# Performance work log

Hardware: AMD Instinct MI355X
Metric: run time of the kernel (lower is better)

Reference implementation:

```python
import jax, jax.numpy as jnp
import numpy as np
from jax import lax

B, N, C = 4, 20000, 256
NUM_VIEW = 300
NUM_SAMPLE = 1024
EPS_BN = 1e-5


def _grasp_views(n=NUM_VIEW):
    # graspnetAPI generate_grasp_views: spiral points on unit sphere
    phi = (np.sqrt(5.0) - 1.0) / 2.0
    i = np.arange(n)
    z = (2.0 * i + 1.0) / n - 1.0
    r = np.sqrt(np.maximum(1.0 - z * z, 0.0))
    x = r * np.cos(2.0 * np.pi * i * phi)
    y = r * np.sin(2.0 * np.pi * i * phi)
    return jnp.asarray(np.stack([x, y, z], axis=1).astype(np.float32))  # [300,3]

_TEMPLATE_VIEWS = _grasp_views()


def _conv1x1(x, w, b):
    # Conv1d with kernel_size=1: x [B,Cin,N], w [Cout,Cin], b [Cout]
    return jnp.einsum('oc,bcn->bon', w, x) + b[None, :, None]


def _bn_eval(x, g, be, m, v):
    # BatchNorm1d in eval mode (running stats)
    scale = g / jnp.sqrt(v + EPS_BN)
    return x * scale[None, :, None] + (be - m * scale)[None, :, None]


def _masked_fps(xyz, mask, n_samples):
    # Equivalent to compacting valid points, running torch furthest_point_sample,
    # and mapping indices back: run FPS on the full set with invalid points pinned
    # to -inf min-distance so they are never selected. Start = first valid index
    # (index 0 of the compacted set). Tie-breaking matches (order preserved).
    first = jnp.argmax(mask, axis=1)                      # [B]
    init_d = jnp.where(mask, jnp.float32(1e10), -jnp.inf)  # [B,N]

    def step(carry, _):
        dists, last = carry
        p = jnp.take_along_axis(xyz, last[:, None, None], axis=1)  # [B,1,3]
        d = jnp.sum((xyz - p) ** 2, axis=-1)                       # [B,N]
        dists = jnp.minimum(dists, d)
        nxt = jnp.argmax(dists, axis=1)
        return (dists, nxt), nxt

    _, rest = lax.scan(step, (init_d, first), None, length=n_samples - 1)
    return jnp.concatenate([first[None, :], rest], axis=0).T  # [B,S] int


def _viewpoint_to_matrix(towards):
    # batch_viewpoint_params_to_matrix with batch_angle = 0 => R1 = I
    ax = towards  # [M,3]
    ay = jnp.stack([-ax[:, 1], ax[:, 0], jnp.zeros_like(ax[:, 0])], axis=-1)
    deg = jnp.sum(ay * ay, axis=-1, keepdims=True) == 0
    ay = jnp.where(deg, jnp.array([0.0, 1.0, 0.0], dtype=ax.dtype), ay)
    nx = ax / jnp.linalg.norm(ax, axis=-1, keepdims=True)
    ny = ay / jnp.linalg.norm(ay, axis=-1, keepdims=True)
    nz = jnp.cross(nx, ny)
    return jnp.stack([nx, ny, nz], axis=-1)  # [M,3,3], axes as columns


def setup_inputs() -> dict:
    key = jax.random.key(0)
    ks = jax.random.split(key, 18)

    def w(k, shape, s=0.05):
        return jax.random.normal(k, shape, jnp.float32) * s

    return dict(
        seed_xyz=jax.random.normal(ks[0], (B, N, 3), jnp.float32),
        seed_features=jax.random.normal(ks[1], (B, C, N), jnp.float32),
        gh_w1=w(ks[2], (C, C)), gh_b1=w(ks[3], (C,), 0.01),
        gh_g=1.0 + 0.1 * jax.random.normal(ks[4], (C,), jnp.float32),
        gh_be=w(ks[5], (C,), 0.01),
        gh_m=w(ks[6], (C,), 0.1),
        gh_v=jax.random.uniform(ks[7], (C,), jnp.float32, 0.5, 1.5),
        gh_w2=w(ks[8], (3, C)), gh_b2=w(ks[9], (3,), 0.01),
        c1_w=w(ks[10], (C, C)), c1_b=w(ks[11], (C,), 0.01),
        bn_g=1.0 + 0.1 * jax.random.normal(ks[12], (C,), jnp.float32),
        bn_b=w(ks[13], (C,), 0.01),
        bn_m=w(ks[14], (C,), 0.1),
        bn_v=jax.random.uniform(ks[15], (C,), jnp.float32, 0.5, 1.5),
        c2_w=w(ks[16], (3, C)), c2_b=w(ks[17], (3,), 0.01),
    )


def reference(seed_xyz, seed_features, gh_w1, gh_b1, gh_g, gh_be, gh_m, gh_v,
              gh_w2, gh_b2, c1_w, c1_b, bn_g, bn_b, bn_m, bn_v, c2_w, c2_b):
    # graspable head: conv-BN-ReLU-conv -> [B,3,N]
    h = jax.nn.relu(_bn_eval(_conv1x1(seed_features, gh_w1, gh_b1), gh_g, gh_be, gh_m, gh_v))
    graspable = _conv1x1(h, gh_w2, gh_b2)
    objectness_score = graspable[:, :2]          # [B,2,N]
    graspness_score = graspable[:, 2]            # [B,N]

    obj_mask = jnp.argmax(objectness_score, axis=1) == 1
    gmask = (graspness_score > 0.1) & obj_mask   # [B,N] bool

    graspable_inds = _masked_fps(seed_xyz, gmask, NUM_SAMPLE)            # [B,S]
    graspable_xyz = jnp.take_along_axis(seed_xyz, graspable_inds[:, :, None], axis=1)   # [B,S,3]
    graspable_features = jnp.take_along_axis(seed_features, graspable_inds[:, None, :], axis=2)  # [B,C,S]
    fp2_graspness = jnp.take_along_axis(graspness_score, graspable_inds, axis=1)        # [B,S]

    f = jax.nn.relu(_bn_eval(_conv1x1(graspable_features, c1_w, c1_b), bn_g, bn_b, bn_m, bn_v))
    vp_xyz = jnp.transpose(_conv1x1(f, c2_w, c2_b), (0, 2, 1))  # [B,S,3]

    # cosine similarity against 300 template views (torch clamps each norm at 1e-8)
    vn = vp_xyz / jnp.maximum(jnp.linalg.norm(vp_xyz, axis=-1, keepdims=True), 1e-8)
    tn = _TEMPLATE_VIEWS / jnp.maximum(jnp.linalg.norm(_TEMPLATE_VIEWS, axis=-1, keepdims=True), 1e-8)
    cos = jnp.einsum('bsd,vd->bsv', vn, tn)      # [B,S,300]
    top_view_inds = jnp.argmax(cos, axis=2)      # [B,S]

    vp_rot = _viewpoint_to_matrix(-vp_xyz.reshape(-1, 3)).reshape(B, NUM_SAMPLE, 3, 3)

    return (objectness_score, graspness_score, graspable_xyz, graspable_inds,
            graspable_features, fp2_graspness, vp_xyz, top_view_inds, vp_rot)
```

## Files before the change

kernel.cpp:

```cpp
#include <hip/hip_runtime.h>
#include <hip/hip_bf16.h>
#include <math.h>

static constexpr int BB = 4;
static constexpr int NN = 20000;
static constexpr int CC = 256;
static constexpr int SS = 1024;
static constexpr int NV = 300;

static constexpr size_t O0 = 0;
static constexpr size_t O1 = O0 + (size_t)BB*2*NN;
static constexpr size_t O2 = O1 + (size_t)BB*NN;
static constexpr size_t O3 = O2 + (size_t)BB*SS*3;
static constexpr size_t O4 = O3 + (size_t)BB*SS;
static constexpr size_t O5 = O4 + (size_t)BB*CC*SS;
static constexpr size_t O6 = O5 + (size_t)BB*SS;
static constexpr size_t O7 = O6 + (size_t)BB*SS*3;
static constexpr size_t O8 = O7 + (size_t)BB*SS;

typedef float v2f __attribute__((ext_vector_type(2)));

static constexpr int KC = 32;
static constexpr int SW_LD = 260;
static constexpr int PS_LD = 68;

static constexpr int G1_TN  = 128;
static constexpr int G1_KC  = 16;
static constexpr int G1_LD  = 260;
static constexpr int G1_BUF = G1_KC*G1_LD + G1_KC*G1_TN;

__global__ __launch_bounds__(256, 2) void gemm_fused(
    const float* __restrict__ X,
    const float* __restrict__ W1, const float* __restrict__ B1v,
    const float* __restrict__ Gv, const float* __restrict__ BEv,
    const float* __restrict__ Mv, const float* __restrict__ Vv,
    const float* __restrict__ W2, const float* __restrict__ B2v,
    float* __restrict__ o0, float* __restrict__ o1)
{
    __shared__ alignas(16) float smem[2*G1_BUF];
    float* psum = smem;

    const int t  = threadIdx.x;
    const int b  = blockIdx.y;
    const int n0 = blockIdx.x * G1_TN;
    const int tm = t & 31;
    const int tj = t >> 5;
    const float* Xb = X + (size_t)b * CC * NN;
    const bool full = (n0 + G1_TN <= NN);

    v2f acc2[8][8];
#pragma unroll
    for (int i = 0; i < 8; ++i)
#pragma unroll
        for (int jp = 0; jp < 8; ++jp) acc2[i][jp] = (v2f){0.f, 0.f};

    float4 wreg[4];
    float4 xr0, xr1;

    auto stage_load = [&](int k0) {
#pragma unroll
        for (int r = 0; r < 4; ++r) {
            int f  = r*1024 + t*4;
            int m  = f >> 4;
            int kk = f & 15;
            wreg[r] = *(const float4*)&W1[(size_t)m*CC + k0 + kk];
        }
        int fx = t*8;
        int kk = fx >> 7;
        int j  = fx & 127;
        if (full) {
            xr0 = *(const float4*)&Xb[(size_t)(k0+kk)*NN + n0 + j];
            xr1 = *(const float4*)&Xb[(size_t)(k0+kk)*NN + n0 + j + 4];
        } else {
            float ta[4], tb[4];
#pragma unroll
            for (int u = 0; u < 4; ++u) {
                int c0 = n0 + j + u;
                int c1 = n0 + j + 4 + u;
                ta[u] = (c0 < NN) ? Xb[(size_t)(k0+kk)*NN + c0] : 0.f;
                tb[u] = (c1 < NN) ? Xb[(size_t)(k0+kk)*NN + c1] : 0.f;
            }
            xr0 = make_float4(ta[0], ta[1], ta[2], ta[3]);
            xr1 = make_float4(tb[0], tb[1], tb[2], tb[3]);
        }
    };

    auto stage_write = [&](float* base) {
        float* sWb = base;
        float* sFb = base + G1_KC*G1_LD;
#pragma unroll
        for (int r = 0; r < 4; ++r) {
            int f  = r*1024 + t*4;
            int m  = f >> 4;
            int kk = f & 15;
            float tmp[4] = {wreg[r].x, wreg[r].y, wreg[r].z, wreg[r].w};
#pragma unroll
            for (int u = 0; u < 4; ++u)
                sWb[(kk+u)*G1_LD + m] = tmp[u];
        }
        int fx = t*8;
        int kk = fx >> 7;
        int j  = fx & 127;
        *(float4*)&sFb[kk*G1_TN + j]     = xr0;
        *(float4*)&sFb[kk*G1_TN + j + 4] = xr1;
    };

    stage_load(0);
    stage_write(smem);
    __syncthreads();

    for (int c = 0; c < CC/G1_KC; ++c) {
        const int cur = c & 1;
        float* base_cur = smem + cur*G1_BUF;
        float* base_nxt = smem + (cur^1)*G1_BUF;

        if (c + 1 < CC/G1_KC) stage_load((c+1)*G1_KC);

        const float* sWc = base_cur;
        const float* sFc = base_cur + G1_KC*G1_LD;
#pragma unroll 8
        for (int kk = 0; kk < G1_KC; ++kk) {
            const float4 a0 = *(const float4*)(sWc + kk*G1_LD + tm*8);
            const float4 a1 = *(const float4*)(sWc + kk*G1_LD + tm*8 + 4);
            const float4 f0 = *(const float4*)(sFc + kk*G1_TN + tj*16);
            const float4 f1 = *(const float4*)(sFc + kk*G1_TN + tj*16 + 4);
            const float4 f2 = *(const float4*)(sFc + kk*G1_TN + tj*16 + 8);
            const float4 f3 = *(const float4*)(sFc + kk*G1_TN + tj*16 + 12);
            float av[8] = {a0.x,a0.y,a0.z,a0.w,a1.x,a1.y,a1.z,a1.w};
            v2f bv2[8] = {{f0.x,f0.y},{f0.z,f0.w},{f1.x,f1.y},{f1.z,f1.w},
                          {f2.x,f2.y},{f2.z,f2.w},{f3.x,f3.y},{f3.z,f3.w}};
#pragma unroll
            for (int i = 0; i < 8; ++i) {
                v2f ai = {av[i], av[i]};
#pragma unroll
                for (int jp = 0; jp < 8; ++jp)
                    acc2[i][jp] += ai * bv2[jp];
            }
        }

        if (c + 1 < CC/G1_KC) stage_write(base_nxt);
        __syncthreads();
    }

    for (int h = 0; h < 2; ++h) {
        if ((tj >> 2) == h) {
            float part[3][16];
#pragma unroll
            for (int r = 0; r < 3; ++r)
#pragma unroll
                for (int j = 0; j < 16; ++j) part[r][j] = 0.f;
#pragma unroll
            for (int i = 0; i < 8; ++i) {
                int m = tm*8 + i;
                float scale = __fdiv_rn(Gv[m], __fsqrt_rn(__fadd_rn(Vv[m], 1e-5f)));
                float shift = __fsub_rn(BEv[m], __fmul_rn(Mv[m], scale));
                float w0 = W2[m], w1 = W2[CC + m], w2 = W2[2*CC + m];
                float b1m = B1v[m];
#pragma unroll
                for (int j = 0; j < 16; ++j) {
                    float x = __fadd_rn(acc2[i][j>>1][j&1], b1m);
                    float y = __fadd_rn(__fmul_rn(x, scale), shift);
                    float hv = y > 0.f ? y : 0.f;
                    part[0][j] = fmaf(w0, hv, part[0][j]);
                    part[1][j] = fmaf(w1, hv, part[1][j]);
                    part[2][j] = fmaf(w2, hv, part[2][j]);
                }
            }
            int tq = tj & 3;
#pragma unroll
            for (int r = 0; r < 3; ++r)
#pragma unroll
                for (int q = 0; q < 4; ++q) {
                    float4 p = {part[r][4*q], part[r][4*q+1], part[r][4*q+2], part[r][4*q+3]};
                    *(float4*)(psum + (r*32 + tm)*PS_LD + tq*16 + q*4) = p;
                }
        }
        __syncthreads();
        if (t < 192) {
            int r = t >> 6, col = t & 63;
            float s = 0.f;
#pragma unroll
            for (int w = 0; w < 32; ++w) s = __fadd_rn(s, psum[(r*32 + w)*PS_LD + col]);
            float tot = __fadd_rn(s, B2v[r]);
            int n = n0 + h*64 + col;
            if (n < NN) {
                if (r == 0)      o0[(size_t)b*2*NN + n]      = tot;
                else if (r == 1) o0[(size_t)b*2*NN + NN + n] = tot;
                else             o1[(size_t)b*NN + n]        = tot;
            }
        }
        __syncthreads();
    }
}

static constexpr int FPS_T = 256;
static constexpr int KAMAX = 20;
static constexpr int CAPA  = FPS_T * KAMAX;

template<int CTRL>
__device__ __forceinline__ unsigned long long dpp_umax(unsigned long long k) {
    int lo = __builtin_amdgcn_update_dpp(0, (int)(unsigned)k,         CTRL, 0xf, 0xf, false);
    int hi = __builtin_amdgcn_update_dpp(0, (int)(unsigned)(k >> 32), CTRL, 0xf, 0xf, false);
    unsigned long long ok = ((unsigned long long)(unsigned)hi << 32) | (unsigned)lo;
    return ok > k ? ok : k;
}

__device__ __forceinline__ unsigned long long wave_umax_dpp(unsigned long long k) {
    k = dpp_umax<0x111>(k);
    k = dpp_umax<0x112>(k);
    k = dpp_umax<0x114>(k);
    k = dpp_umax<0x118>(k);
    k = dpp_umax<0x142>(k);
    k = dpp_umax<0x143>(k);
    return k;
}

__device__ __forceinline__ unsigned long long pack_key(float v, int i) {
    unsigned long long k = (((unsigned long long)__float_as_uint(v)) << 32)
                         | (unsigned long long)(0xFFFFFFFFu - (unsigned)i);
    return (v == -INFINITY) ? 0ull : k;
}

template<int KP>
__device__ __forceinline__ void fps_scan_loop(
    int cnt, const float* __restrict__ sxyz,
    unsigned long long (*swk)[4], int* __restrict__ whist)
{
#pragma clang fp contract(off)
    const int t = threadIdx.x;
    const int wave = t >> 6, lane = t & 63;

    v2f X2[KP], Y2[KP], Z2[KP], D2[KP];
#pragma unroll
    for (int jp = 0; jp < KP; ++jp) {
        int g0 = t + ((2*jp) << 8);
        int g1 = g0 + 256;
        bool v0 = g0 < cnt, v1 = g1 < cnt;
        float4 wa = v0 ? *(const float4*)&sxyz[g0*4] : make_float4(0.f,0.f,0.f,0.f);
        float4 wb = v1 ? *(const float4*)&sxyz[g1*4] : make_float4(0.f,0.f,0.f,0.f);
        X2[jp][0] = wa.x; X2[jp][1] = wb.x;
        Y2[jp][0] = wa.y; Y2[jp][1] = wb.y;
        Z2[jp][0] = wa.z; Z2[jp][1] = wb.z;
        D2[jp][0] = v0 ? 1e10f : -INFINITY;
        D2[jp][1] = v1 ? 1e10f : -INFINITY;
    }

    float px = sxyz[0], py = sxyz[1], pz = sxyz[2];

    for (int it = 1; it < SS; ++it) {
        float bv = -INFINITY; int bi = 0x7fffffff;
#pragma unroll
        for (int jp = 0; jp < KP; ++jp) {
            v2f dx = X2[jp] - px;
            v2f dy = Y2[jp] - py;
            v2f dz = Z2[jp] - pz;
            v2f xx = dx*dx, yy = dy*dy;
            v2f sxy = xx + yy;
            v2f zz = dz*dz;
            v2f dd = sxy + zz;
            float dn0 = fminf(D2[jp][0], dd[0]);
            float dn1 = fminf(D2[jp][1], dd[1]);
            D2[jp][0] = dn0;
            D2[jp][1] = dn1;
            if (dn0 > bv) { bv = dn0; bi = t + ((2*jp)   << 8); }
            if (dn1 > bv) { bv = dn1; bi = t + ((2*jp+1) << 8); }
        }
        unsigned long long key = wave_umax_dpp(pack_key(bv, bi));
        int par = it & 1;
        if (lane == 63) swk[par][wave] = key;
        __syncthreads();
        const ulonglong2* kp = (const ulonglong2*)&swk[par][0];
        ulonglong2 kA = kp[0], kB = kp[1];
        unsigned long long m0 = kA.x > kA.y ? kA.x : kA.y;
        unsigned long long m1 = kB.x > kB.y ? kB.x : kB.y;
        unsigned long long best = m0 > m1 ? m0 : m1;
        int wi = (int)(0xFFFFFFFFu - (unsigned)(best & 0xFFFFFFFFull));
        float4 w4 = *(const float4*)&sxyz[wi*4];
        px = w4.x; py = w4.y; pz = w4.z;
        if (t == 0) whist[it] = wi;
    }
}

__global__ __launch_bounds__(256, 1) void mega_kernel(
    const float* __restrict__ xyz, const float* __restrict__ feats,
    const float* __restrict__ o0, const float* __restrict__ o1,
    const float* __restrict__ c1w, const float* __restrict__ c1b,
    const float* __restrict__ bng, const float* __restrict__ bnb,
    const float* __restrict__ bnm, const float* __restrict__ bnv,
    const float* __restrict__ c2w, const float* __restrict__ c2b,
    int* __restrict__ corig, float* __restrict__ cxg,
    float* __restrict__ cyg, float* __restrict__ czg,
    float* __restrict__ o2, float* __restrict__ o3, float* __restrict__ o4,
    float* __restrict__ o5, float* __restrict__ o6, float* __restrict__ o7,
    float* __restrict__ o8, int* __restrict__ indsp, int* __restrict__ donep)
{
    __shared__ alignas(16) char sm[86272];
    const int t = threadIdx.x;
    const int wave = t >> 6, lane = t & 63;

    if (blockIdx.x < BB) {
        const int b = blockIdx.x;
        const size_t bofs = (size_t)b*NN;
        float* sxyz = (float*)sm;
        int*   whist = (int*)(sm + 81920);
        unsigned long long (*swk)[4] = (unsigned long long (*)[4])(sm + 86016);
        int*   wsum  = (int*)(sm + 86080);
        int*   smisc = (int*)(sm + 86096);

        if (t == 0) smisc[0] = 0;
        __syncthreads();
        const float* ob0 = o0 + (size_t)b*2*NN;
        const float* ob1 = o1 + (size_t)b*NN;
        for (int base = 0; base < NN; base += 256) {
            int i = base + t;
            bool valid = i < NN;
            float g1 = valid ? ob1[i]      : 0.f;
            float v0 = valid ? ob0[i]      : 0.f;
            float v1 = valid ? ob0[NN + i] : 0.f;
            bool m = valid && (g1 > 0.1f) && (v1 > v0);
            unsigned long long bal = __ballot(m);
            int pre = __popcll(bal & ((1ull << lane) - 1ull));
            if (lane == 0) wsum[wave] = __popcll(bal);
            __syncthreads();
            int offs = smisc[0];
            int tilesum = wsum[0] + wsum[1] + wsum[2] + wsum[3];
            for (int ww = 0; ww < wave; ++ww) offs += wsum[ww];
            if (m) {
                int pos = offs + pre;
                float x = xyz[(bofs + i)*3 + 0];
                float y = xyz[(bofs + i)*3 + 1];
                float z = xyz[(bofs + i)*3 + 2];
                corig[bofs + pos] = i;
                cxg[bofs + pos] = x; cyg[bofs + pos] = y; czg[bofs + pos] = z;
                if (pos < CAPA) {
                    float4 w4 = {x, y, z, 0.f};
                    *(float4*)&sxyz[pos*4] = w4;
                }
            }
            __syncthreads();
            if (t == 0) smisc[0] += tilesum;
        }
        __syncthreads();
        const int cnt = smisc[0];

        float* o3b = o3 + (size_t)b*SS;
        int*   oib = indsp + (size_t)b*SS;

        if (cnt <= 0) {
            for (int s = t; s < SS; s += FPS_T) { o3b[s] = 0.f; oib[s] = 0; }
            __syncthreads();
            if (t == 0) {
                __threadfence();
                __hip_atomic_fetch_add(donep, 1, __ATOMIC_RELEASE, __HIP_MEMORY_SCOPE_AGENT);
            }
            return;
        }

        if (t == 0) whist[0] = 0;
        __syncthreads();

        if (cnt <= CAPA) {
            int kat2 = ((cnt + 255) >> 8);
            kat2 = (kat2 + 1) & ~1;
            int kpn = kat2 >> 1;
            switch (kpn) {
                case 1:  fps_scan_loop<1 >(cnt, sxyz, swk, whist); break;
                case 2:  fps_scan_loop<2 >(cnt, sxyz, swk, whist); break;
                case 3:  fps_scan_loop<3 >(cnt, sxyz, swk, whist); break;
                case 4:  fps_scan_loop<4 >(cnt, sxyz, swk, whist); break;
                case 5:  fps_scan_loop<5 >(cnt, sxyz, swk, whist); break;
                case 6:  fps_scan_loop<6 >(cnt, sxyz, swk, whist); break;
                case 7:  fps_scan_loop<7 >(cnt, sxyz, swk, whist); break;
                case 8:  fps_scan_loop<8 >(cnt, sxyz, swk, whist); break;
                case 9:  fps_scan_loop<9 >(cnt, sxyz, swk, whist); break;
                default: fps_scan_loop<10>(cnt, sxyz, swk, whist); break;
            }
        } else {
            float* Dl = sxyz;
            for (int g = t; g < cnt; g += FPS_T) Dl[g] = 1e10f;
            __syncthreads();
            float px = cxg[bofs], py = cyg[bofs], pz = czg[bofs];
            for (int it = 1; it < SS; ++it) {
                float bv = -INFINITY; int bi = 0x7fffffff;
                for (int g = t; g < cnt; g += FPS_T) {
                    float dx = __fsub_rn(cxg[bofs + g], px);
                    float dy = __fsub_rn(cyg[bofs + g], py);
                    float dz = __fsub_rn(czg[bofs + g], pz);
                    float d  = __fadd_rn(__fadd_rn(__fmul_rn(dx,dx), __fmul_rn(dy,dy)), __fmul_rn(dz,dz));
                    float dn = fminf(Dl[g], d);
                    Dl[g] = dn;
                    if (dn > bv) { bv = dn; bi = g; }
                }
                unsigned long long key = wave_umax_dpp(pack_key(bv, bi));
                int par = it & 1;
                if (lane == 63) swk[par][wave] = key;
                __syncthreads();
                const ulonglong2* kp = (const ulonglong2*)&swk[par][0];
                ulonglong2 kA = kp[0], kB = kp[1];
                unsigned long long m0 = kA.x > kA.y ? kA.x : kA.y;
                unsigned long long m1 = kB.x > kB.y ? kB.x : kB.y;
                unsigned long long best = m0 > m1 ? m0 : m1;
                int wi = (int)(0xFFFFFFFFu - (unsigned)(best & 0xFFFFFFFFull));
                px = cxg[bofs + wi]; py = cyg[bofs + wi]; pz = czg[bofs + wi];
                if (t == 0) whist[it] = wi;
            }
        }

        __syncthreads();
        for (int s = t; s < SS; s += FPS_T) {
            int wi  = whist[s];
            int org = corig[bofs + wi];
            oib[s] = org;
            o3b[s] = (float)org;
        }
        __syncthreads();
        if (t == 0) {
            __threadfence();
            __hip_atomic_fetch_add(donep, 1, __ATOMIC_RELEASE, __HIP_MEMORY_SCOPE_AGENT);
        }
        return;
    }

    const int wid = blockIdx.x - BB;

    float4 g2w[4];
    if (wid < 64) {
#pragma unroll
        for (int r = 0; r < 4; ++r) {
            int f  = r*1024 + t*4;
            int m  = f >> 4;
            int kk = f & 15;
            g2w[r] = *(const float4*)&c1w[(size_t)m*CC + kk];
        }
    }

    {
        int* smisc = (int*)(sm + 86096);
        if (t == 0) smisc[1] = 0;
        __syncthreads();
        float a = 1.0f + (float)t * 1e-6f, bmul = 1.0000001f, c = 0.f;
        for (int iter = 0; iter < (1 << 22); ++iter) {
#pragma unroll
            for (int u = 0; u < 16; ++u) c = fmaf(a, bmul, c);
            __builtin_amdgcn_s_sleep(8);
            if (t == 0 && (iter & 7) == 0) {
                if (__hip_atomic_load(donep, __ATOMIC_RELAXED, __HIP_MEMORY_SCOPE_AGENT) >= BB)
                    *(volatile int*)&smisc[1] = 1;
            }
            if (*(volatile int*)&smisc[1]) break;
        }
        ((volatile float*)(sm + 86144))[t & 31] = c;
        __syncthreads();
        (void)__hip_atomic_load(donep, __ATOMIC_ACQUIRE, __HIP_MEMORY_SCOPE_AGENT);
    }

    if (wid < 64) {
        const int bi = wid >> 4;
        const int n0 = (wid & 15) << 6;
        constexpr int G2_KC  = 16;
        constexpr int G2_LD  = 260;
        constexpr int G2_TN  = 64;
        constexpr int G2_BUF = G2_KC*G2_LD + G2_KC*G2_TN;

        float* smf  = (float*)sm;
        float* psum = smf;
        float* gout = (float*)(sm + 3*32*PS_LD*4);
        float* tv   = (float*)(sm + KC*SW_LD*4);

        const int tm  = t & 31;
        const int tn  = t >> 5;
        const int kk0 = t >> 4;
        const int j0  = (t*4) & 63;

        const int4 sidx4 = *(const int4*)&indsp[(bi << 10) + n0 + j0];
        const size_t frow_base = (size_t)bi * CC;

        v2f acc2[8][4];
#pragma unroll
        for (int i = 0; i < 8; ++i)
#pragma unroll
            for (int jp = 0; jp < 4; ++jp) acc2[i][jp] = (v2f){0.f, 0.f};

        float4 wreg[4] = {g2w[0], g2w[1], g2w[2], g2w[3]};
        float4 xreg;

        auto loadW = [&](int k0) {
#pragma unroll
            for (int r = 0; r < 4; ++r) {
                int f  = r*1024 + t*4;
                int m  = f >> 4;
                int kk = f & 15;
                wreg[r] = *(const float4*)&c1w[(size_t)m*CC + k0 + kk];
            }
        };
        auto loadF = [&](int k0) {
            const float* fb = feats + (frow_base + k0 + kk0)*NN;
            xreg.x = fb[sidx4.x];
            xreg.y = fb[sidx4.y];
            xreg.z = fb[sidx4.z];
            xreg.w = fb[sidx4.w];
        };
        auto stage_write = [&](float* base) {
            float* sWb = base;
            float* sFb = base + G2_KC*G2_LD;
#pragma unroll
            for (int r = 0; r < 4; ++r) {
                int f  = r*1024 + t*4;
                int m  = f >> 4;
                int kk = f & 15;
                float tmp[4] = {wreg[r].x, wreg[r].y, wreg[r].z, wreg[r].w};
#pragma unroll
                for (int u = 0; u < 4; ++u)
                    sWb[(kk+u)*G2_LD + m] = tmp[u];
            }
            *(float4*)&sFb[kk0*G2_TN + j0] = xreg;
        };

        loadF(0);
        stage_write(smf);
        __syncthreads();

        for (int c = 0; c < CC/G2_KC; ++c) {
            const int cur = c & 1;
            float* bcur = smf + cur*G2_BUF;
            float* bnxt = smf + (cur^1)*G2_BUF;

            if (c + 1 < CC/G2_KC) { loadW((c+1)*G2_KC); loadF((c+1)*G2_KC); }

            const float* sWc = bcur;
            const float* sFc = bcur + G2_KC*G2_LD;
#pragma unroll 8
            for (int kk = 0; kk < G2_KC; ++kk) {
                const float4 a0 = *(const float4*)(sWc + kk*G2_LD + tm*8);
                const float4 a1 = *(const float4*)(sWc + kk*G2_LD + tm*8 + 4);
                const float4 f0 = *(const float4*)(sFc + kk*G2_TN + tn*8);
                const float4 f1 = *(const float4*)(sFc + kk*G2_TN + tn*8 + 4);
                float av[8] = {a0.x,a0.y,a0.z,a0.w,a1.x,a1.y,a1.z,a1.w};
                v2f bv2[4] = {{f0.x,f0.y},{f0.z,f0.w},{f1.x,f1.y},{f1.z,f1.w}};
#pragma unroll
                for (int i = 0; i < 8; ++i) {
                    v2f ai = {av[i], av[i]};
#pragma unroll
                    for (int jp = 0; jp < 4; ++jp)
                        acc2[i][jp] += ai * bv2[jp];
                }
            }

            if (c + 1 < CC/G2_KC) stage_write(bnxt);
            __syncthreads();
        }

        float part[3][8];
#pragma unroll
        for (int r = 0; r < 3; ++r)
#pragma unroll
            for (int j = 0; j < 8; ++j) part[r][j] = 0.f;

#pragma unroll
        for (int i = 0; i < 8; ++i) {
            int m = tm*8 + i;
            float scale = __fdiv_rn(bng[m], __fsqrt_rn(__fadd_rn(bnv[m], 1e-5f)));
            float shift = __fsub_rn(bnb[m], __fmul_rn(bnm[m], scale));
            float w0 = c2w[m], w1 = c2w[CC + m], w2 = c2w[2*CC + m];
            float b1m = c1b[m];
#pragma unroll
            for (int j = 0; j < 8; ++j) {
                float x = __fadd_rn(acc2[i][j>>1][j&1], b1m);
                float y = __fadd_rn(__fmul_rn(x, scale), shift);
                float h = y > 0.f ? y : 0.f;
                part[0][j] = fmaf(w0, h, part[0][j]);
                part[1][j] = fmaf(w1, h, part[1][j]);
                part[2][j] = fmaf(w2, h, part[2][j]);
            }
        }
#pragma unroll
        for (int r = 0; r < 3; ++r) {
            float4 p0 = {part[r][0], part[r][1], part[r][2], part[r][3]};
            float4 p1 = {part[r][4], part[r][5], part[r][6], part[r][7]};
            *(float4*)(psum + (r*32 + tm)*PS_LD + tn*8)     = p0;
            *(float4*)(psum + (r*32 + tm)*PS_LD + tn*8 + 4) = p1;
        }
        __syncthreads();
        if (t < 192) {
            int r = t >> 6, col = t & 63;
            float s = 0.f;
#pragma unroll
            for (int w = 0; w < 32; ++w) s = __fadd_rn(s, psum[(r*32 + w)*PS_LD + col]);
            float tot = __fadd_rn(s, c2b[r]);
            gout[r*64 + col] = tot;
            o6[((size_t)bi*SS + n0 + col)*3 + r] = tot;
        }
        __syncthreads();
        for (int i = t; i < NV; i += 256) {
            double phi = (sqrt(5.0) - 1.0) * 0.5;
            double zd  = (2.0*(double)i + 1.0)/300.0 - 1.0;
            double rr  = sqrt(fmax(1.0 - zd*zd, 0.0));
            double ang = 2.0 * 3.14159265358979323846 * (double)i * phi;
            float fx = (float)(rr * cos(ang));
            float fy = (float)(rr * sin(ang));
            float fz = (float)zd;
            float nr = __fsqrt_rn(__fadd_rn(__fadd_rn(__fmul_rn(fx,fx), __fmul_rn(fy,fy)), __fmul_rn(fz,fz)));
            float dn = fmaxf(nr, 1e-8f);
            tv[i]       = __fdiv_rn(fx, dn);
            tv[NV + i]  = __fdiv_rn(fy, dn);
            tv[2*NV + i]= __fdiv_rn(fz, dn);
        }
        __syncthreads();
        if (t < 64) {
            int col = t;
            int sg = bi*SS + n0 + col;
            float vx = gout[col], vy = gout[64 + col], vz = gout[128 + col];

            float nr = __fsqrt_rn(__fadd_rn(__fadd_rn(__fmul_rn(vx,vx), __fmul_rn(vy,vy)), __fmul_rn(vz,vz)));
            float dn = fmaxf(nr, 1e-8f);
            float ux = __fdiv_rn(vx, dn), uy = __fdiv_rn(vy, dn), uz = __fdiv_rn(vz, dn);
            float best = -INFINITY; int bidx = 0;
            for (int v = 0; v < NV; ++v) {
                float cde = __fadd_rn(__fadd_rn(__fmul_rn(ux, tv[v]), __fmul_rn(uy, tv[NV+v])), __fmul_rn(uz, tv[2*NV+v]));
                if (cde > best) { best = cde; bidx = v; }
            }
            o7[sg] = (float)bidx;

            float axx = -vx, axy = -vy, axz = -vz;
            float ayx = vy, ayy = -vx, ayz = 0.f;
            float s2 = __fadd_rn(__fadd_rn(__fmul_rn(ayx,ayx), __fmul_rn(ayy,ayy)), 0.f);
            if (s2 == 0.f) { ayx = 0.f; ayy = 1.f; ayz = 0.f; }
            float an = __fsqrt_rn(__fadd_rn(__fadd_rn(__fmul_rn(axx,axx), __fmul_rn(axy,axy)), __fmul_rn(axz,axz)));
            float nx0 = __fdiv_rn(axx, an), nx1 = __fdiv_rn(axy, an), nx2 = __fdiv_rn(axz, an);
            float bn2 = __fsqrt_rn(__fadd_rn(__fadd_rn(__fmul_rn(ayx,ayx), __fmul_rn(ayy,ayy)), __fmul_rn(ayz,ayz)));
            float ny0 = __fdiv_rn(ayx, bn2), ny1 = __fdiv_rn(ayy, bn2), ny2 = __fdiv_rn(ayz, bn2);
            float nz0 = __fsub_rn(__fmul_rn(nx1, ny2), __fmul_rn(nx2, ny1));
            float nz1 = __fsub_rn(__fmul_rn(nx2, ny0), __fmul_rn(nx0, ny2));
            float nz2 = __fsub_rn(__fmul_rn(nx0, ny1), __fmul_rn(nx1, ny0));
            size_t o = (size_t)sg * 9;
            o8[o+0] = nx0; o8[o+1] = ny0; o8[o+2] = nz0;
            o8[o+3] = nx1; o8[o+4] = ny1; o8[o+5] = nz1;
            o8[o+6] = nx2; o8[o+7] = ny2; o8[o+8] = nz2;
        }
    } else {
        const int NQ = (BB*CC*SS) / 4;
        for (int q = (wid - 64)*256 + t; q < NQ; q += 188*256) {
            int e = q << 2;
            int b = e >> 18;
            int r = e & ((1 << 18) - 1);
            int c = r >> 10;
            int s = r & 1023;
            int4 i4 = *(const int4*)&indsp[(b << 10) + s];
            const float* fb = feats + ((size_t)b*CC + c)*NN;
            float4 v = { fb[i4.x], fb[i4.y], fb[i4.z], fb[i4.w] };
            *(float4*)&o4[e] = v;
            if (c == 0) {
                const float* gb = o1 + (size_t)b*NN;
                float4 g4 = { gb[i4.x], gb[i4.y], gb[i4.z], gb[i4.w] };
                *(float4*)&o5[(b << 10) + s] = g4;
                const float* xb = xyz + (size_t)b*NN*3;
                float o2buf[12];
                int ii[4] = { i4.x, i4.y, i4.z, i4.w };
#pragma unroll
                for (int k = 0; k < 4; ++k) {
                    o2buf[k*3+0] = xb[(size_t)ii[k]*3 + 0];
                    o2buf[k*3+1] = xb[(size_t)ii[k]*3 + 1];
                    o2buf[k*3+2] = xb[(size_t)ii[k]*3 + 2];
                }
                float* dst = o2 + ((size_t)(b << 10) + s)*3;
                *(float4*)&dst[0] = *(float4*)&o2buf[0];
                *(float4*)&dst[4] = *(float4*)&o2buf[4];
                *(float4*)&dst[8] = *(float4*)&o2buf[8];
            }
        }
    }
}

extern "C" void kernel_launch(void* const* d_in, const int* in_sizes, int n_in,
                              void* d_out, int out_size, void* d_ws, size_t ws_size,
                              hipStream_t stream) {
    const float* xyz   = (const float*)d_in[0];
    const float* feats = (const float*)d_in[1];
    const float* gh_w1 = (const float*)d_in[2];
    const float* gh_b1 = (const float*)d_in[3];
    const float* gh_g  = (const float*)d_in[4];
    const float* gh_be = (const float*)d_in[5];
    const float* gh_m  = (const float*)d_in[6];
    const float* gh_v  = (const float*)d_in[7];
    const float* gh_w2 = (const float*)d_in[8];
    const float* gh_b2 = (const float*)d_in[9];
    const float* c1_w  = (const float*)d_in[10];
    const float* c1_b  = (const float*)d_in[11];
    const float* bn_g  = (const float*)d_in[12];
    const float* bn_b  = (const float*)d_in[13];
    const float* bn_m  = (const float*)d_in[14];
    const float* bn_v  = (const float*)d_in[15];
    const float* c2_w  = (const float*)d_in[16];
    const float* c2_b  = (const float*)d_in[17];

    float* out = (float*)d_out;
    float* o0 = out + O0;
    float* o1 = out + O1;
    float* o2 = out + O2;
    float* o3 = out + O3;
    float* o4 = out + O4;
    float* o5 = out + O5;
    float* o6 = out + O6;
    float* o7 = out + O7;
    float* o8 = out + O8;

    char* ws = (char*)d_ws;
    size_t off = 0;
    auto take = [&](size_t bytes) -> char* {
        char* p = ws + off;
        off = (off + bytes + 255) & ~(size_t)255;
        return p;
    };
    int*   corig = (int*)take((size_t)BB*NN*4);
    float* cx    = (float*)take((size_t)BB*NN*4);
    float* cy    = (float*)take((size_t)BB*NN*4);
    float* cz    = (float*)take((size_t)BB*NN*4);
    int*   indsp = (int*)take((size_t)BB*SS*4);
    int*   donep = (int*)take(64);

    gemm_fused<<<dim3((NN + G1_TN - 1)/G1_TN, BB), 256, 0, stream>>>(
        feats, gh_w1, gh_b1, gh_g, gh_be, gh_m, gh_v, gh_w2, gh_b2, o0, o1);

    hipMemsetAsync(donep, 0, 4, stream);
    mega_kernel<<<dim3(256), 256, 0, stream>>>(
        xyz, feats, o0, o1,
        c1_w, c1_b, bn_g, bn_b, bn_m, bn_v, c2_w, c2_b,
        corig, cx, cy, cz,
        o2, o3, o4, o5, o6, o7, o8, indsp, donep);
}
```

Before: 960.5 us.

## Stream FPS progress in 256-sample chunks so consumers overlap FPS; halve GEMM tile

The FPS blocks now publish selected indices every 256 iterations through a per-batch progress counter, replacing a single global done flag. Head and gather blocks wait only for the chunk they need, so the conv head and the feature gather can overlap the serial FPS loop instead of waiting for all of it to finish. Separately, the first GEMM tile width is halved from 128 to 64 columns, which doubles the grid and simplifies the epilogue. The risks are extra syncthreads and global stores inside the FPS loop, more spin-wait polling, and a smaller per-block register tile in the GEMM.

```diff
diff --git a/kernel.cpp b/kernel.cpp
--- a/kernel.cpp
+++ b/kernel.cpp
@@ -24,7 +24,7 @@
 static constexpr int SW_LD = 260;
 static constexpr int PS_LD = 68;
 
-static constexpr int G1_TN  = 128;
+static constexpr int G1_TN  = 64;
 static constexpr int G1_KC  = 16;
 static constexpr int G1_LD  = 260;
 static constexpr int G1_BUF = G1_KC*G1_LD + G1_KC*G1_TN;
@@ -39,23 +39,24 @@
 {
     __shared__ alignas(16) float smem[2*G1_BUF];
     float* psum = smem;
+    float* gout = smem + 3*32*PS_LD;
 
     const int t  = threadIdx.x;
     const int b  = blockIdx.y;
     const int n0 = blockIdx.x * G1_TN;
     const int tm = t & 31;
-    const int tj = t >> 5;
+    const int tn = t >> 5;
     const float* Xb = X + (size_t)b * CC * NN;
     const bool full = (n0 + G1_TN <= NN);
 
-    v2f acc2[8][8];
+    v2f acc2[8][4];
 #pragma unroll
     for (int i = 0; i < 8; ++i)
 #pragma unroll
-        for (int jp = 0; jp < 8; ++jp) acc2[i][jp] = (v2f){0.f, 0.f};
+        for (int jp = 0; jp < 4; ++jp) acc2[i][jp] = (v2f){0.f, 0.f};
 
     float4 wreg[4];
-    float4 xr0, xr1;
+    float4 xreg;
 
     auto stage_load = [&](int k0) {
 #pragma unroll
@@ -65,29 +66,23 @@
             int kk = f & 15;
             wreg[r] = *(const float4*)&W1[(size_t)m*CC + k0 + kk];
         }
-        int fx = t*8;
-        int kk = fx >> 7;
-        int j  = fx & 127;
+        int fx = t*4;
+        int kk = fx >> 6;
+        int j  = fx & 63;
         if (full) {
-            xr0 = *(const float4*)&Xb[(size_t)(k0+kk)*NN + n0 + j];
-            xr1 = *(const float4*)&Xb[(size_t)(k0+kk)*NN + n0 + j + 4];
+            xreg = *(const float4*)&Xb[(size_t)(k0+kk)*NN + n0 + j];
         } else {
-            float ta[4], tb[4];
+            float tmp[4];
 #pragma unroll
             for (int u = 0; u < 4; ++u) {
-                int c0 = n0 + j + u;
-                int c1 = n0 + j + 4 + u;
-                ta[u] = (c0 < NN) ? Xb[(size_t)(k0+kk)*NN + c0] : 0.f;
-                tb[u] = (c1 < NN) ? Xb[(size_t)(k0+kk)*NN + c1] : 0.f;
-            }
-            xr0 = make_float4(ta[0], ta[1], ta[2], ta[3]);
-            xr1 = make_float4(tb[0], tb[1], tb[2], tb[3]);
+                int col = n0 + j + u;
+                tmp[u] = (col < NN) ? Xb[(size_t)(k0+kk)*NN + col] : 0.f;
+            }
+            xreg = make_float4(tmp[0], tmp[1], tmp[2], tmp[3]);
         }
     };
 
-    auto stage_write = [&](float* base) {
-        float* sWb = base;
-        float* sFb = base + G1_KC*G1_LD;
+    auto stage_write = [&](float* sWb, float* sFb) {
 #pragma unroll
         for (int r = 0; r < 4; ++r) {
             int f  = r*1024 + t*4;
@@ -98,15 +93,14 @@
             for (int u = 0; u < 4; ++u)
                 sWb[(kk+u)*G1_LD + m] = tmp[u];
         }
-        int fx = t*8;
-        int kk = fx >> 7;
-        int j  = fx & 127;
-        *(float4*)&sFb[kk*G1_TN + j]     = xr0;
-        *(float4*)&sFb[kk*G1_TN + j + 4] = xr1;
+        int fx = t*4;
+        int kk = fx >> 6;
+        int j  = fx & 63;
+        *(float4*)&sFb[kk*G1_TN + j] = xreg;
     };
 
     stage_load(0);
-    stage_write(smem);
+    stage_write(smem, smem + G1_KC*G1_LD);
     __syncthreads();
 
     for (int c = 0; c < CC/G1_KC; ++c) {
@@ -122,74 +116,70 @@
         for (int kk = 0; kk < G1_KC; ++kk) {
             const float4 a0 = *(const float4*)(sWc + kk*G1_LD + tm*8);
             const float4 a1 = *(const float4*)(sWc + kk*G1_LD + tm*8 + 4);
-            const float4 f0 = *(const float4*)(sFc + kk*G1_TN + tj*16);
-            const float4 f1 = *(const float4*)(sFc + kk*G1_TN + tj*16 + 4);
-            const float4 f2 = *(const float4*)(sFc + kk*G1_TN + tj*16 + 8);
-            const float4 f3 = *(const float4*)(sFc + kk*G1_TN + tj*16 + 12);
+            const float4 f0 = *(const float4*)(sFc + kk*G1_TN + tn*8);
+            const float4 f1 = *(const float4*)(sFc + kk*G1_TN + tn*8 + 4);
             float av[8] = {a0.x,a0.y,a0.z,a0.w,a1.x,a1.y,a1.z,a1.w};
-            v2f bv2[8] = {{f0.x,f0.y},{f0.z,f0.w},{f1.x,f1.y},{f1.z,f1.w},
-                          {f2.x,f2.y},{f2.z,f2.w},{f3.x,f3.y},{f3.z,f3.w}};
+            v2f bv2[4] = {{f0.x,f0.y},{f0.z,f0.w},{f1.x,f1.y},{f1.z,f1.w}};
 #pragma unroll
             for (int i = 0; i < 8; ++i) {
                 v2f ai = {av[i], av[i]};
 #pragma unroll
-                for (int jp = 0; jp < 8; ++jp)
+                for (int jp = 0; jp < 4; ++jp)
                     acc2[i][jp] += ai * bv2[jp];
             }
         }
 
-        if (c + 1 < CC/G1_KC) stage_write(base_nxt);
-        __syncthreads();
-    }
-
-    for (int h = 0; h < 2; ++h) {
-        if ((tj >> 2) == h) {
-            float part[3][16];
-#pragma unroll
-            for (int r = 0; r < 3; ++r)
-#pragma unroll
-                for (int j = 0; j < 16; ++j) part[r][j] = 0.f;
-#pragma unroll
-            for (int i = 0; i < 8; ++i) {
-                int m = tm*8 + i;
-                float scale = __fdiv_rn(Gv[m], __fsqrt_rn(__fadd_rn(Vv[m], 1e-5f)));
-                float shift = __fsub_rn(BEv[m], __fmul_rn(Mv[m], scale));
-                float w0 = W2[m], w1 = W2[CC + m], w2 = W2[2*CC + m];
-                float b1m = B1v[m];
-#pragma unroll
-                for (int j = 0; j < 16; ++j) {
-                    float x = __fadd_rn(acc2[i][j>>1][j&1], b1m);
-                    float y = __fadd_rn(__fmul_rn(x, scale), shift);
-                    float hv = y > 0.f ? y : 0.f;
-                    part[0][j] = fmaf(w0, hv, part[0][j]);
-                    part[1][j] = fmaf(w1, hv, part[1][j]);
-                    part[2][j] = fmaf(w2, hv, part[2][j]);
-                }
-            }
-            int tq = tj & 3;
-#pragma unroll
-            for (int r = 0; r < 3; ++r)
-#pragma unroll
-                for (int q = 0; q < 4; ++q) {
-                    float4 p = {part[r][4*q], part[r][4*q+1], part[r][4*q+2], part[r][4*q+3]};
-                    *(float4*)(psum + (r*32 + tm)*PS_LD + tq*16 + q*4) = p;
-                }
-        }
-        __syncthreads();
-        if (t < 192) {
-            int r = t >> 6, col = t & 63;
-            float s = 0.f;
-#pragma unroll
-            for (int w = 0; w < 32; ++w) s = __fadd_rn(s, psum[(r*32 + w)*PS_LD + col]);
-            float tot = __fadd_rn(s, B2v[r]);
-            int n = n0 + h*64 + col;
-            if (n < NN) {
-                if (r == 0)      o0[(size_t)b*2*NN + n]      = tot;
-                else if (r == 1) o0[(size_t)b*2*NN + NN + n] = tot;
-                else             o1[(size_t)b*NN + n]        = tot;
-            }
-        }
-        __syncthreads();
+        if (c + 1 < CC/G1_KC) stage_write(base_nxt, base_nxt + G1_KC*G1_LD);
+        __syncthreads();
+    }
+
+    float part[3][8];
+#pragma unroll
+    for (int r = 0; r < 3; ++r)
+#pragma unroll
+        for (int j = 0; j < 8; ++j) part[r][j] = 0.f;
+
+#pragma unroll
+    for (int i = 0; i < 8; ++i) {
+        int m = tm*8 + i;
+        float scale = __fdiv_rn(Gv[m], __fsqrt_rn(__fadd_rn(Vv[m], 1e-5f)));
+        float shift = __fsub_rn(BEv[m], __fmul_rn(Mv[m], scale));
+        float w0 = W2[m], w1 = W2[CC + m], w2 = W2[2*CC + m];
+        float b1m = B1v[m];
+#pragma unroll
+        for (int j = 0; j < 8; ++j) {
+            float x = __fadd_rn(acc2[i][j>>1][j&1], b1m);
+            float y = __fadd_rn(__fmul_rn(x, scale), shift);
+            float h = y > 0.f ? y : 0.f;
+            part[0][j] = fmaf(w0, h, part[0][j]);
+            part[1][j] = fmaf(w1, h, part[1][j]);
+            part[2][j] = fmaf(w2, h, part[2][j]);
+        }
+    }
+#pragma unroll
+    for (int r = 0; r < 3; ++r) {
+        float4 p0 = {part[r][0], part[r][1], part[r][2], part[r][3]};
+        float4 p1 = {part[r][4], part[r][5], part[r][6], part[r][7]};
+        *(float4*)(psum + (r*32 + tm)*PS_LD + tn*8)     = p0;
+        *(float4*)(psum + (r*32 + tm)*PS_LD + tn*8 + 4) = p1;
+    }
+    __syncthreads();
+    if (t < 192) {
+        int r = t >> 6, col = t & 63;
+        float s = 0.f;
+#pragma unroll
+        for (int w = 0; w < 32; ++w) s = __fadd_rn(s, psum[(r*32 + w)*PS_LD + col]);
+        float tot = __fadd_rn(s, B2v[r]);
+        gout[r*64 + col] = tot;
+    }
+    __syncthreads();
+    if (t < 64) {
+        int n = n0 + t;
+        if (n < NN) {
+            o0[(size_t)b*2*NN + n]      = gout[t];
+            o0[(size_t)b*2*NN + NN + n] = gout[64 + t];
+            o1[(size_t)b*NN + n]        = gout[128 + t];
+        }
     }
 }
 
@@ -221,10 +211,29 @@
     return (v == -INFINITY) ? 0ull : k;
 }
 
+__device__ __forceinline__ void fps_publish(
+    int hi, const int* __restrict__ whist, const int* __restrict__ corig_b,
+    int* __restrict__ oib, float* __restrict__ o3b, int* __restrict__ progb)
+{
+    const int t = threadIdx.x;
+    int s = hi - 256 + t;
+    int wi  = whist[s];
+    int org = corig_b[wi];
+    oib[s] = org;
+    o3b[s] = (float)org;
+    __syncthreads();
+    if (t == 0) {
+        __threadfence();
+        __hip_atomic_store(progb, hi, __ATOMIC_RELEASE, __HIP_MEMORY_SCOPE_AGENT);
+    }
+}
+
 template<int KP>
 __device__ __forceinline__ void fps_scan_loop(
     int cnt, const float* __restrict__ sxyz,
-    unsigned long long (*swk)[4], int* __restrict__ whist)
+    unsigned long long (*swk)[4], int* __restrict__ whist,
+    const int* __restrict__ corig_b, int* __restrict__ oib,
+    float* __restrict__ o3b, int* __restrict__ progb)
 {
 #pragma clang fp contract(off)
     const int t = threadIdx.x;
@@ -278,6 +287,8 @@
         float4 w4 = *(const float4*)&sxyz[wi*4];
         px = w4.x; py = w4.y; pz = w4.z;
         if (t == 0) whist[it] = wi;
+        if ((it & 255) == 0)
+            fps_publish(it, whist, corig_b, oib, o3b, progb);
     }
 }
 
@@ -292,7 +303,7 @@
     float* __restrict__ cyg, float* __restrict__ czg,
     float* __restrict__ o2, float* __restrict__ o3, float* __restrict__ o4,
     float* __restrict__ o5, float* __restrict__ o6, float* __restrict__ o7,
-    float* __restrict__ o8, int* __restrict__ indsp, int* __restrict__ donep)
+    float* __restrict__ o8, int* __restrict__ indsp, int* __restrict__ progp)
 {
     __shared__ alignas(16) char sm[86272];
     const int t = threadIdx.x;
@@ -351,29 +362,32 @@
             __syncthreads();
             if (t == 0) {
                 __threadfence();
-                __hip_atomic_fetch_add(donep, 1, __ATOMIC_RELEASE, __HIP_MEMORY_SCOPE_AGENT);
+                __hip_atomic_store(progp + b, SS, __ATOMIC_RELEASE, __HIP_MEMORY_SCOPE_AGENT);
             }
             return;
         }
 
         if (t == 0) whist[0] = 0;
         __syncthreads();
+
+        const int* corig_b = corig + bofs;
+        int* progb = progp + b;
 
         if (cnt <= CAPA) {
             int kat2 = ((cnt + 255) >> 8);
             kat2 = (kat2 + 1) & ~1;
             int kpn = kat2 >> 1;
             switch (kpn) {
-                case 1:  fps_scan_loop<1 >(cnt, sxyz, swk, whist); break;
-                case 2:  fps_scan_loop<2 >(cnt, sxyz, swk, whist); break;
-                case 3:  fps_scan_loop<3 >(cnt, sxyz, swk, whist); break;
-                case 4:  fps_scan_loop<4 >(cnt, sxyz, swk, whist); break;
-                case 5:  fps_scan_loop<5 >(cnt, sxyz, swk, whist); break;
-                case 6:  fps_scan_loop<6 >(cnt, sxyz, swk, whist); break;
-                case 7:  fps_scan_loop<7 >(cnt, sxyz, swk, whist); break;
-                case 8:  fps_scan_loop<8 >(cnt, sxyz, swk, whist); break;
-                case 9:  fps_scan_loop<9 >(cnt, sxyz, swk, whist); break;
-                default: fps_scan_loop<10>(cnt, sxyz, swk, whist); break;
+                case 1:  fps_scan_loop<1 >(cnt, sxyz, swk, whist, corig_b, oib, o3b, progb); break;
+                case 2:  fps_scan_loop<2 >(cnt, sxyz, swk, whist, corig_b, oib, o3b, progb); break;
+                case 3:  fps_scan_loop<3 >(cnt, sxyz, swk, whist, corig_b, oib, o3b, progb); break;
+                case 4:  fps_scan_loop<4 >(cnt, sxyz, swk, whist, corig_b, oib, o3b, progb); break;
+                case 5:  fps_scan_loop<5 >(cnt, sxyz, swk, whist, corig_b, oib, o3b, progb); break;
+                case 6:  fps_scan_loop<6 >(cnt, sxyz, swk, whist, corig_b, oib, o3b, progb); break;
+                case 7:  fps_scan_loop<7 >(cnt, sxyz, swk, whist, corig_b, oib, o3b, progb); break;
+                case 8:  fps_scan_loop<8 >(cnt, sxyz, swk, whist, corig_b, oib, o3b, progb); break;
+                case 9:  fps_scan_loop<9 >(cnt, sxyz, swk, whist, corig_b, oib, o3b, progb); break;
+                default: fps_scan_loop<10>(cnt, sxyz, swk, whist, corig_b, oib, o3b, progb); break;
             }
         } else {
             float* Dl = sxyz;
@@ -403,28 +417,67 @@
                 int wi = (int)(0xFFFFFFFFu - (unsigned)(best & 0xFFFFFFFFull));
                 px = cxg[bofs + wi]; py = cyg[bofs + wi]; pz = czg[bofs + wi];
                 if (t == 0) whist[it] = wi;
-            }
-        }
-
-        __syncthreads();
-        for (int s = t; s < SS; s += FPS_T) {
-            int wi  = whist[s];
-            int org = corig[bofs + wi];
-            oib[s] = org;
-            o3b[s] = (float)org;
-        }
+                if ((it & 255) == 0)
+                    fps_publish(it, whist, corig_b, oib, o3b, progb);
+            }
+        }
+
+        __syncthreads();
+        fps_publish(SS, whist, corig_b, oib, o3b, progb);
+        return;
+    }
+
+    const int wid = blockIdx.x - BB;
+    volatile int* fl = (volatile int*)(sm + 86096);
+
+    auto wait_prog = [&](int bsel, int thr, bool all4) {
         __syncthreads();
         if (t == 0) {
-            __threadfence();
-            __hip_atomic_fetch_add(donep, 1, __ATOMIC_RELEASE, __HIP_MEMORY_SCOPE_AGENT);
-        }
-        return;
-    }
-
-    const int wid = blockIdx.x - BB;
-
-    float4 g2w[4];
+            bool ok;
+            if (all4) {
+                ok = (__hip_atomic_load(&progp[0], __ATOMIC_RELAXED, __HIP_MEMORY_SCOPE_AGENT) >= thr)
+                  && (__hip_atomic_load(&progp[1], __ATOMIC_RELAXED, __HIP_MEMORY_SCOPE_AGENT) >= thr)
+                  && (__hip_atomic_load(&progp[2], __ATOMIC_RELAXED, __HIP_MEMORY_SCOPE_AGENT) >= thr)
+                  && (__hip_atomic_load(&progp[3], __ATOMIC_RELAXED, __HIP_MEMORY_SCOPE_AGENT) >= thr);
+            } else {
+                ok = (__hip_atomic_load(&progp[bsel], __ATOMIC_RELAXED, __HIP_MEMORY_SCOPE_AGENT) >= thr);
+            }
+            *fl = ok ? 1 : 0;
+        }
+        __syncthreads();
+        if (!*fl) {
+            float a = 1.0f + (float)t * 1e-6f, bmul = 1.0000001f, c = 0.f;
+            for (int iter = 0; iter < (1 << 22); ++iter) {
+#pragma unroll
+                for (int u = 0; u < 16; ++u) c = fmaf(a, bmul, c);
+                __builtin_amdgcn_s_sleep(8);
+                if (t == 0 && (iter & 7) == 0) {
+                    bool ok;
+                    if (all4) {
+                        ok = (__hip_atomic_load(&progp[0], __ATOMIC_RELAXED, __HIP_MEMORY_SCOPE_AGENT) >= thr)
+                          && (__hip_atomic_load(&progp[1], __ATOMIC_RELAXED, __HIP_MEMORY_SCOPE_AGENT) >= thr)
+                          && (__hip_atomic_load(&progp[2], __ATOMIC_RELAXED, __HIP_MEMORY_SCOPE_AGENT) >= thr)
+                          && (__hip_atomic_load(&progp[3], __ATOMIC_RELAXED, __HIP_MEMORY_SCOPE_AGENT) >= thr);
+                    } else {
+                        ok = (__hip_atomic_load(&progp[bsel], __ATOMIC_RELAXED, __HIP_MEMORY_SCOPE_AGENT) >= thr);
+                    }
+                    if (ok) *fl = 1;
+                }
+                if (*fl) break;
+            }
+            ((volatile float*)(sm + 86144))[t & 31] = c;
+            __syncthreads();
+        }
+#pragma unroll
+        for (int bq = 0; bq < BB; ++bq)
+            (void)__hip_atomic_load(&progp[bq], __ATOMIC_ACQUIRE, __HIP_MEMORY_SCOPE_AGENT);
+    };
+
     if (wid < 64) {
+        const int bi = wid >> 4;
+        const int n0 = (wid & 15) << 6;
+
+        float4 g2w[4];
 #pragma unroll
         for (int r = 0; r < 4; ++r) {
             int f  = r*1024 + t*4;
@@ -432,31 +485,9 @@
             int kk = f & 15;
             g2w[r] = *(const float4*)&c1w[(size_t)m*CC + kk];
         }
-    }
-
-    {
-        int* smisc = (int*)(sm + 86096);
-        if (t == 0) smisc[1] = 0;
-        __syncthreads();
-        float a = 1.0f + (float)t * 1e-6f, bmul = 1.0000001f, c = 0.f;
-        for (int iter = 0; iter < (1 << 22); ++iter) {
-#pragma unroll
-            for (int u = 0; u < 16; ++u) c = fmaf(a, bmul, c);
-            __builtin_amdgcn_s_sleep(8);
-            if (t == 0 && (iter & 7) == 0) {
-                if (__hip_atomic_load(donep, __ATOMIC_RELAXED, __HIP_MEMORY_SCOPE_AGENT) >= BB)
-                    *(volatile int*)&smisc[1] = 1;
-            }
-            if (*(volatile int*)&smisc[1]) break;
-        }
-        ((volatile float*)(sm + 86144))[t & 31] = c;
-        __syncthreads();
-        (void)__hip_atomic_load(donep, __ATOMIC_ACQUIRE, __HIP_MEMORY_SCOPE_AGENT);
-    }
-
-    if (wid < 64) {
-        const int bi = wid >> 4;
-        const int n0 = (wid & 15) << 6;
+
+        wait_prog(bi, n0 + 64, false);
+
         constexpr int G2_KC  = 16;
         constexpr int G2_LD  = 260;
         constexpr int G2_TN  = 64;
@@ -638,34 +669,38 @@
             o8[o+6] = nx2; o8[o+7] = ny2; o8[o+8] = nz2;
         }
     } else {
-        const int NQ = (BB*CC*SS) / 4;
-        for (int q = (wid - 64)*256 + t; q < NQ; q += 188*256) {
-            int e = q << 2;
-            int b = e >> 18;
-            int r = e & ((1 << 18) - 1);
-            int c = r >> 10;
-            int s = r & 1023;
-            int4 i4 = *(const int4*)&indsp[(b << 10) + s];
-            const float* fb = feats + ((size_t)b*CC + c)*NN;
-            float4 v = { fb[i4.x], fb[i4.y], fb[i4.z], fb[i4.w] };
-            *(float4*)&o4[e] = v;
-            if (c == 0) {
-                const float* gb = o1 + (size_t)b*NN;
-                float4 g4 = { gb[i4.x], gb[i4.y], gb[i4.z], gb[i4.w] };
-                *(float4*)&o5[(b << 10) + s] = g4;
-                const float* xb = xyz + (size_t)b*NN*3;
-                float o2buf[12];
-                int ii[4] = { i4.x, i4.y, i4.z, i4.w };
-#pragma unroll
-                for (int k = 0; k < 4; ++k) {
-                    o2buf[k*3+0] = xb[(size_t)ii[k]*3 + 0];
-                    o2buf[k*3+1] = xb[(size_t)ii[k]*3 + 1];
-                    o2buf[k*3+2] = xb[(size_t)ii[k]*3 + 2];
+        const int gw = wid - 64;
+        for (int k = 0; k < 4; ++k) {
+            wait_prog(0, (k + 1) << 8, true);
+            const int NQc = (BB*CC*256) / 4;
+            for (int qq = gw*256 + t; qq < NQc; qq += 188*256) {
+                int e = qq << 2;
+                int b = e >> 16;
+                int r = e & 65535;
+                int c = r >> 8;
+                int s = (k << 8) + (r & 255);
+                int4 i4 = *(const int4*)&indsp[(b << 10) + s];
+                const float* fb = feats + ((size_t)b*CC + c)*NN;
+                float4 v = { fb[i4.x], fb[i4.y], fb[i4.z], fb[i4.w] };
+                *(float4*)&o4[(((size_t)b*CC + c) << 10) + s] = v;
+                if (c == 0) {
+                    const float* gb = o1 + (size_t)b*NN;
+                    float4 g4 = { gb[i4.x], gb[i4.y], gb[i4.z], gb[i4.w] };
+                    *(float4*)&o5[(b << 10) + s] = g4;
+                    const float* xb = xyz + (size_t)b*NN*3;
+                    float o2buf[12];
+                    int ii[4] = { i4.x, i4.y, i4.z, i4.w };
+#pragma unroll
+                    for (int kq = 0; kq < 4; ++kq) {
+                        o2buf[kq*3+0] = xb[(size_t)ii[kq]*3 + 0];
+                        o2buf[kq*3+1] = xb[(size_t)ii[kq]*3 + 1];
+                        o2buf[kq*3+2] = xb[(size_t)ii[kq]*3 + 2];
+                    }
+                    float* dst = o2 + ((size_t)(b << 10) + s)*3;
+                    *(float4*)&dst[0] = *(float4*)&o2buf[0];
+                    *(float4*)&dst[4] = *(float4*)&o2buf[4];
+                    *(float4*)&dst[8] = *(float4*)&o2buf[8];
                 }
-                float* dst = o2 + ((size_t)(b << 10) + s)*3;
-                *(float4*)&dst[0] = *(float4*)&o2buf[0];
-                *(float4*)&dst[4] = *(float4*)&o2buf[4];
-                *(float4*)&dst[8] = *(float4*)&o2buf[8];
             }
         }
     }
@@ -716,15 +751,15 @@
     float* cy    = (float*)take((size_t)BB*NN*4);
     float* cz    = (float*)take((size_t)BB*NN*4);
     int*   indsp = (int*)take((size_t)BB*SS*4);
-    int*   donep = (int*)take(64);
+    int*   progp = (int*)take(64);
 
     gemm_fused<<<dim3((NN + G1_TN - 1)/G1_TN, BB), 256, 0, stream>>>(
         feats, gh_w1, gh_b1, gh_g, gh_be, gh_m, gh_v, gh_w2, gh_b2, o0, o1);
 
-    hipMemsetAsync(donep, 0, 4, stream);
+    hipMemsetAsync(progp, 0, 16, stream);
     mega_kernel<<<dim3(256), 256, 0, stream>>>(
         xyz, feats, o0, o1,
         c1_w, c1_b, bn_g, bn_b, bn_m, bn_v, c2_w, c2_b,
         corig, cx, cy, cz,
-        o2, o3, o4, o5, o6, o7, o8, indsp, donep);
+        o2, o3, o4, o5, o6, o7, o8, indsp, progp);
 }
```

New measurement: 953.6 us. Within noise of the previous version (-0.7%).
